# Kernel optimization log

Measured on AMD Instinct MI355X. Metric: run time of the kernel, lower is better.

The kernel has to match this reference:

```python
import jax, jax.numpy as jnp
import numpy as np

D = 1024
H = 16
HD = D // H
EPS = 1e-6


def setup_inputs() -> dict:
    key = jax.random.key(0)
    ks = jax.random.split(key, 10)
    s = 1.0 / np.sqrt(D)
    inp = {
        "x": jax.random.normal(ks[0], (2, 2048, D), dtype=jnp.float32),
        "Wq": jax.random.uniform(ks[1], (D, D), jnp.float32, -s, s),
        "bq": jax.random.uniform(ks[2], (D,), jnp.float32, -s, s),
        "Wk": jax.random.uniform(ks[3], (D, D), jnp.float32, -s, s),
        "bk": jax.random.uniform(ks[4], (D,), jnp.float32, -s, s),
        "Wv": jax.random.uniform(ks[5], (D, D), jnp.float32, -s, s),
        "bv": jax.random.uniform(ks[6], (D,), jnp.float32, -s, s),
        "Wo": jax.random.uniform(ks[7], (D, D), jnp.float32, -s, s),
        "bo": jax.random.uniform(ks[8], (D,), jnp.float32, -s, s),
        "gamma": jnp.ones((D,), jnp.float32),
        "beta": jnp.zeros((D,), jnp.float32),
    }
    return inp


def _mha(x, Wq, bq, Wk, bk, Wv, bv, Wo, bo, gamma, beta):
    B, S, _ = x.shape
    # Linear projections (torch Linear: x @ W.T + b), split heads -> [B,H,S,hd]
    q = (x @ Wq.T + bq).reshape(B, S, H, HD).transpose(0, 2, 1, 3)
    k = (x @ Wk.T + bk).reshape(B, S, H, HD).transpose(0, 2, 1, 3)
    v = (x @ Wv.T + bv).reshape(B, S, H, HD).transpose(0, 2, 1, 3)
    scores = jnp.einsum("bhqd,bhkd->bhqk", q, k) / jnp.sqrt(jnp.float32(HD))
    attn = jax.nn.softmax(scores, axis=-1)
    ctx = jnp.einsum("bhqk,bhkd->bhqd", attn, v)
    ctx = ctx.transpose(0, 2, 1, 3).reshape(B, S, D)
    out = ctx @ Wo.T + bo  # dropout p=0.0 -> identity
    res = x + out
    mu = jnp.mean(res, axis=-1, keepdims=True)
    var = jnp.mean(jnp.square(res - mu), axis=-1, keepdims=True)
    return (res - mu) / jnp.sqrt(var + EPS) * gamma + beta


def reference(x, Wq, bq, Wk, bk, Wv, bv, Wo, bo, gamma, beta):
    return _mha(x, Wq, bq, Wk, bk, Wv, bv, Wo, bo, gamma, beta)
```

## Files before the change

### kernel.cpp

```cpp
#include <hip/hip_runtime.h>
#include <hip/hip_bf16.h>
#include <math.h>

#define D_MODEL 1024
#define NH 16
#define HDIM 64
#define BB 2
#define SS 2048
#define MTOK (BB*SS)

typedef __hip_bfloat16 bf16;
typedef short s8v __attribute__((ext_vector_type(8)));
typedef float f4v __attribute__((ext_vector_type(4)));
typedef float f16v __attribute__((ext_vector_type(16)));

__device__ __forceinline__ float bf2f(bf16 x) { return __bfloat162float(x); }
__device__ __forceinline__ bf16 f2bf(float x) { return __float2bfloat16(x); }

typedef const __attribute__((address_space(1))) unsigned int* gas_u32;
typedef __attribute__((address_space(3))) unsigned int* las_u32;
#define ASYNC16(gp, lp) __builtin_amdgcn_global_load_lds((gas_u32)(gp), (las_u32)(lp), 16, 0, 0)

#define QSCALE 0.18033688f

__device__ __forceinline__ unsigned int cvtpk_bf16(float a, float b) {
    unsigned int r;
    asm("v_cvt_pk_bf16_f32 %0, %1, %2" : "=v"(r) : "v"(a), "v"(b));
    return r;
}

__global__ __launch_bounds__(256)
void cvt_kernel(const float* __restrict__ x,  const float* __restrict__ wq,
                const float* __restrict__ wk, const float* __restrict__ wv,
                const float* __restrict__ wo, bf16* __restrict__ dst)
{
    const size_t e = ((size_t)blockIdx.x * 256 + threadIdx.x) * 4;
    const size_t M1 = (size_t)1 << 20;
    const float* src; size_t off;
    if      (e < 4 * M1) { src = x;  off = e;          }
    else if (e < 5 * M1) { src = wq; off = e - 4 * M1; }
    else if (e < 6 * M1) { src = wk; off = e - 5 * M1; }
    else if (e < 7 * M1) { src = wv; off = e - 6 * M1; }
    else                 { src = wo; off = e - 7 * M1; }
    const float4 v = *(const float4*)&src[off];
    bf16 h[4] = { f2bf(v.x), f2bf(v.y), f2bf(v.z), f2bf(v.w) };
    *(uint2*)&dst[e] = *(const uint2*)h;
}

__global__ __launch_bounds__(256, 2)
void gemm_qkv(const bf16* __restrict__ X,
              const bf16* __restrict__ Wq, const float* __restrict__ bq,
              const bf16* __restrict__ Wk, const float* __restrict__ bk,
              const bf16* __restrict__ Wv, const float* __restrict__ bv,
              bf16* __restrict__ q_ws, bf16* __restrict__ k_ws, bf16* __restrict__ v_ws)
{
    const int mat = blockIdx.z;
    const bf16*  W    = (mat == 0) ? Wq : ((mat == 1) ? Wk : Wv);
    const float* bias = (mat == 0) ? bq : ((mat == 1) ? bk : bv);

    const int t = threadIdx.x;
    const int lane = t & 63, wave = t >> 6;
    const int wrow = wave >> 1, wcol = wave & 1;
    const int quad = lane >> 4, l15 = lane & 15;

    const bf16 *Ap, *Bp; int m0, n0;
    if (mat < 2) { Ap = X; Bp = W; m0 = blockIdx.y * 128; n0 = blockIdx.x * 128; }
    else         { Ap = W; Bp = X; m0 = blockIdx.x * 128; n0 = blockIdx.y * 128; }

    __shared__ __align__(16) bf16 As[128 * 64];
    __shared__ __align__(16) bf16 Bs[128 * 64];

    f4v acc[4][4];
#pragma unroll
    for (int i = 0; i < 4; i++)
#pragma unroll
        for (int j = 0; j < 4; j++) acc[i][j] = (f4v){0.f, 0.f, 0.f, 0.f};

    for (int kk = 0; kk < D_MODEL; kk += 64) {
#pragma unroll
        for (int p = 0; p < 4; p++) {
            const int c = p * 256 + t;
            const int row = c >> 3, j = c & 7;
            ASYNC16(&Ap[(size_t)(m0 + row) * D_MODEL + kk + (j ^ (row & 7)) * 8], &As[c * 8]);
        }
#pragma unroll
        for (int p = 0; p < 4; p++) {
            const int c = p * 256 + t;
            const int row = c >> 3, j = c & 7;
            ASYNC16(&Bp[(size_t)(n0 + row) * D_MODEL + kk + (j ^ (row & 7)) * 8], &Bs[c * 8]);
        }
        __syncthreads();

#pragma unroll
        for (int ks = 0; ks < 2; ks++) {
            s8v af[4], bf_[4];
#pragma unroll
            for (int i = 0; i < 4; i++) {
                const int row = wrow * 64 + i * 16 + l15;
                const int g = (ks * 4 + quad) ^ (row & 7);
                af[i] = *(const s8v*)&As[row * 64 + g * 8];
            }
#pragma unroll
            for (int j = 0; j < 4; j++) {
                const int row = wcol * 64 + j * 16 + l15;
                const int g = (ks * 4 + quad) ^ (row & 7);
                bf_[j] = *(const s8v*)&Bs[row * 64 + g * 8];
            }
#pragma unroll
            for (int i = 0; i < 4; i++)
#pragma unroll
                for (int j = 0; j < 4; j++)
                    acc[i][j] = __builtin_amdgcn_mfma_f32_16x16x32_bf16(af[i], bf_[j], acc[i][j], 0, 0, 0);
        }
        __syncthreads();
    }

    if (mat == 2) {
#pragma unroll
        for (int i = 0; i < 4; i++) {
#pragma unroll
            for (int r = 0; r < 4; r++) {
                const int f = m0 + wrow * 64 + i * 16 + quad * 4 + r;
                const float bv_ = bias[f];
#pragma unroll
                for (int j = 0; j < 4; j++) {
                    const int tok = n0 + wcol * 64 + j * 16 + l15;
                    const int b = tok >> 11, s = tok & 2047;
                    v_ws[((size_t)(b * D_MODEL + f)) * SS + s] = f2bf(acc[i][j][r] + bv_);
                }
            }
        }
    } else {
        bf16* dst = (mat == 0) ? q_ws : k_ws;
        const float scale = (mat == 0) ? QSCALE : 1.0f;
#pragma unroll
        for (int j = 0; j < 4; j++) {
            const int col = n0 + wcol * 64 + j * 16 + l15;
            const float bv_ = bias[col];
            const int h = col >> 6, hd = col & 63;
#pragma unroll
            for (int i = 0; i < 4; i++) {
#pragma unroll
                for (int r = 0; r < 4; r++) {
                    const int row = m0 + wrow * 64 + i * 16 + quad * 4 + r;
                    const int b = row >> 11, s = row & 2047;
                    const float v = (acc[i][j][r] + bv_) * scale;
                    dst[(((size_t)(b * NH + h)) * SS + s) * HDIM + hd] = f2bf(v);
                }
            }
        }
    }
}

__device__ __forceinline__ f16v qk_tile(const bf16* Ksc, const s8v* qf,
                                        const int mt, const int l31, const int L5)
{
    f16v sc;
#pragma unroll
    for (int i = 0; i < 16; i++) sc[i] = 0.f;
    __builtin_amdgcn_s_setprio(1);
#pragma unroll
    for (int kc = 0; kc < 4; kc++) {
        const int g = (kc * 2 + L5) ^ (l31 & 7);
        const s8v kf = *(const s8v*)&Ksc[(mt * 32 + l31) * 64 + g * 8];
        sc = __builtin_amdgcn_mfma_f32_32x32x16_bf16(kf, qf[kc], sc, 0, 0, 0);
    }
    __builtin_amdgcn_s_setprio(0);
    return sc;
}

__global__ __launch_bounds__(512, 4)
void attn_kernel(const bf16* __restrict__ Q, const bf16* __restrict__ K,
                 const bf16* __restrict__ VtG, bf16* __restrict__ ctx)
{
    const int s_ = blockIdx.x;
    const int lb = (s_ & 7) * 64 + (s_ >> 3);
    const int bh = lb >> 4;
    const int q0 = (lb & 15) * 128;
    const bf16* Qp = Q   + (size_t)bh * SS * HDIM;
    const bf16* Kp = K   + (size_t)bh * SS * HDIM;
    const bf16* Vp = VtG + (size_t)bh * HDIM * SS;

    __shared__ __align__(16) bf16 Qs[128 * 64];
    __shared__ __align__(16) bf16 Ks[2][128 * 64];
    __shared__ __align__(16) bf16 Vt[2][64 * 128];

    const int t = threadIdx.x;
    const int lane = t & 63, wave = t >> 6;
    const int l31 = lane & 31, L5 = lane >> 5;
    const int qb = (wave & 3) * 32;
    const int half = wave >> 2;

    const int vrbase = t >> 4;
    const int vcol = (t & 15) * 8;
    uint4 vv[2];
#pragma unroll
    for (int p = 0; p < 2; p++)
        vv[p] = *(const uint4*)&Vp[(size_t)(p * 32 + vrbase) * SS + vcol];
#pragma unroll
    for (int p = 0; p < 2; p++) {
        const int c = p * 512 + t;
        const int row = c >> 3, j = c & 7;
        ASYNC16(&Kp[(size_t)row * HDIM + (j ^ (row & 7)) * 8], &Ks[0][c * 8]);
    }
#pragma unroll
    for (int p = 0; p < 2; p++) {
        const int c = p * 512 + t;
        const int row = c >> 3, g = (c & 7) ^ (row & 7);
        *(uint4*)&Qs[row * 64 + g * 8] = *(const uint4*)&Qp[(size_t)(q0 + row) * HDIM + (c & 7) * 8];
    }
    const int cA = vcol,     pA = (cA & ~12) | ((cA & 4) << 1) | ((cA & 8) >> 1);
    const int cB = vcol + 4, pB = (cB & ~12) | ((cB & 4) << 1) | ((cB & 8) >> 1);
    {
        union { uint4 u4; uint2 u2[2]; } uu;
#pragma unroll
        for (int p = 0; p < 2; p++) {
            const int vr = p * 32 + vrbase;
            uu.u4 = vv[p];
            *(uint2*)&Vt[0][vr * 128 + (((pA >> 3) ^ (vr & 15)) * 8) + (pA & 7)] = uu.u2[0];
            *(uint2*)&Vt[0][vr * 128 + (((pB >> 3) ^ (vr & 15)) * 8) + (pB & 7)] = uu.u2[1];
        }
    }
    __syncthreads();

    s8v qf[4];
#pragma unroll
    for (int kc = 0; kc < 4; kc++) {
        const int g = (kc * 2 + L5) ^ (l31 & 7);
        qf[kc] = *(const s8v*)&Qs[(qb + l31) * 64 + g * 8];
    }

    float l_own = 0.f;
    f16v o_acc[2];
#pragma unroll
    for (int i = 0; i < 16; i++) { o_acc[0][i] = 0.f; o_acc[1][i] = 0.f; }

    int cur = 0;
    for (int it = 0; it < SS / 128; ++it) {
        const bool have = (it < SS / 128 - 1);
        const int s0n = (it + 1) * 128;

        uint4 nv0, nv1;
        if (have) {
            nv0 = *(const uint4*)&Vp[(size_t)(vrbase) * SS + s0n + vcol];
            nv1 = *(const uint4*)&Vp[(size_t)(32 + vrbase) * SS + s0n + vcol];
#pragma unroll
            for (int p = 0; p < 2; p++) {
                const int c = p * 512 + t;
                const int row = c >> 3, j = c & 7;
                ASYNC16(&Kp[(size_t)(s0n + row) * HDIM + (j ^ (row & 7)) * 8],
                        &Ks[cur ^ 1][c * 8]);
            }
        }

        const bf16* Ksc = &Ks[cur][0];
        const bf16* Vtc = &Vt[cur][0];
#pragma unroll
        for (int mt2 = 0; mt2 < 2; mt2++) {
            const int mt = half * 2 + mt2;
            f16v sc = qk_tile(Ksc, qf, mt, l31, L5);
            float tps = 0.f;
#pragma unroll
            for (int i = 0; i < 16; i++) { sc[i] = __builtin_amdgcn_exp2f(sc[i]); tps += sc[i]; }
            l_own += tps;
            unsigned int pk[8];
#pragma unroll
            for (int i = 0; i < 8; i++) pk[i] = cvtpk_bf16(sc[2 * i], sc[2 * i + 1]);
            __builtin_amdgcn_s_setprio(1);
#pragma unroll
            for (int c = 0; c < 2; c++) {
                const s8v pf = *(const s8v*)&pk[c * 4];
#pragma unroll
                for (int dt = 0; dt < 2; dt++) {
                    const int g = (mt * 4 + c * 2 + L5) ^ (l31 & 15);
                    const s8v vf = *(const s8v*)&Vtc[(dt * 32 + l31) * 128 + g * 8];
                    o_acc[dt] = __builtin_amdgcn_mfma_f32_32x32x16_bf16(pf, vf, o_acc[dt], 0, 0, 0);
                }
            }
            __builtin_amdgcn_s_setprio(0);
        }

        if (have) {
            bf16* VtN = &Vt[cur ^ 1][0];
            union { uint4 u4; uint2 u2[2]; } uu;
            const int vr0 = vrbase, vr1 = 32 + vrbase;
            uu.u4 = nv0;
            *(uint2*)&VtN[vr0 * 128 + (((pA >> 3) ^ (vr0 & 15)) * 8) + (pA & 7)] = uu.u2[0];
            *(uint2*)&VtN[vr0 * 128 + (((pB >> 3) ^ (vr0 & 15)) * 8) + (pB & 7)] = uu.u2[1];
            uu.u4 = nv1;
            *(uint2*)&VtN[vr1 * 128 + (((pA >> 3) ^ (vr1 & 15)) * 8) + (pA & 7)] = uu.u2[0];
            *(uint2*)&VtN[vr1 * 128 + (((pB >> 3) ^ (vr1 & 15)) * 8) + (pB & 7)] = uu.u2[1];
        }
        __syncthreads();
        cur ^= 1;
    }

    const float l_wave = l_own + __shfl_xor(l_own, 32);
    float* o_sh = (float*)&Ks[0][0];
    float* l_sh = (float*)&Vt[0][0];
    if (half == 1) {
        const int pr = wave & 3;
#pragma unroll
        for (int dt = 0; dt < 2; dt++)
#pragma unroll
            for (int reg = 0; reg < 16; reg++)
                o_sh[((pr * 2 + dt) * 16 + reg) * 64 + lane] = o_acc[dt][reg];
        if (lane < 32) l_sh[pr * 32 + l31] = l_wave;
    }
    __syncthreads();
    if (half == 0) {
        const int pr = wave;
        const float linv = 1.0f / (l_wave + l_sh[pr * 32 + l31]);
        const int b = bh >> 4, h = bh & 15;
#pragma unroll
        for (int reg = 0; reg < 16; reg++) {
            const int R = (reg & 3) + 8 * (reg >> 2) + 4 * L5;
            const float lr = __shfl(linv, R);
            const int tok = q0 + qb + R;
            const size_t rb = ((size_t)(b * SS + tok)) * D_MODEL + h * 64;
#pragma unroll
            for (int dt = 0; dt < 2; dt++) {
                const float val = o_acc[dt][reg] + o_sh[((pr * 2 + dt) * 16 + reg) * 64 + lane];
                ctx[rb + dt * 32 + l31] = f2bf(val * lr);
            }
        }
    }
}

__global__ __launch_bounds__(256, 2)
void gemm_oproj(const bf16* __restrict__ Ctx, const bf16* __restrict__ Wo,
                const float* __restrict__ bo, const float* __restrict__ X,
                float* __restrict__ res)
{
    const int m0 = blockIdx.y * 128, n0 = blockIdx.x * 128;
    const int t = threadIdx.x;
    const int lane = t & 63, wave = t >> 6;
    const int wrow = wave >> 1, wcol = wave & 1;
    const int quad = lane >> 4, l15 = lane & 15;

    __shared__ __align__(16) bf16 As[128 * 64];
    __shared__ __align__(16) bf16 Bs[128 * 64];

    f4v acc[4][4];
#pragma unroll
    for (int i = 0; i < 4; i++)
#pragma unroll
        for (int j = 0; j < 4; j++) acc[i][j] = (f4v){0.f, 0.f, 0.f, 0.f};

    for (int kk = 0; kk < D_MODEL; kk += 64) {
#pragma unroll
        for (int p = 0; p < 4; p++) {
            const int c = p * 256 + t;
            const int row = c >> 3, j = c & 7;
            ASYNC16(&Ctx[(size_t)(m0 + row) * D_MODEL + kk + (j ^ (row & 7)) * 8], &As[c * 8]);
        }
#pragma unroll
        for (int p = 0; p < 4; p++) {
            const int c = p * 256 + t;
            const int row = c >> 3, j = c & 7;
            ASYNC16(&Wo[(size_t)(n0 + row) * D_MODEL + kk + (j ^ (row & 7)) * 8], &Bs[c * 8]);
        }
        __syncthreads();

#pragma unroll
        for (int ks = 0; ks < 2; ks++) {
            s8v af[4], bf_[4];
#pragma unroll
            for (int i = 0; i < 4; i++) {
                const int row = wrow * 64 + i * 16 + l15;
                const int g = (ks * 4 + quad) ^ (row & 7);
                af[i] = *(const s8v*)&As[row * 64 + g * 8];
            }
#pragma unroll
            for (int j = 0; j < 4; j++) {
                const int row = wcol * 64 + j * 16 + l15;
                const int g = (ks * 4 + quad) ^ (row & 7);
                bf_[j] = *(const s8v*)&Bs[row * 64 + g * 8];
            }
#pragma unroll
            for (int i = 0; i < 4; i++)
#pragma unroll
                for (int j = 0; j < 4; j++)
                    acc[i][j] = __builtin_amdgcn_mfma_f32_16x16x32_bf16(af[i], bf_[j], acc[i][j], 0, 0, 0);
        }
        __syncthreads();
    }

#pragma unroll
    for (int j = 0; j < 4; j++) {
        const int col = n0 + wcol * 64 + j * 16 + l15;
        const float bv_ = bo[col];
#pragma unroll
        for (int i = 0; i < 4; i++) {
#pragma unroll
            for (int r = 0; r < 4; r++) {
                const int row = m0 + wrow * 64 + i * 16 + quad * 4 + r;
                const size_t idx = (size_t)row * D_MODEL + col;
                res[idx] = acc[i][j][r] + bv_ + X[idx];
            }
        }
    }
}

__global__ __launch_bounds__(256)
void ln_kernel(const float* __restrict__ res, const float* __restrict__ gamma,
               const float* __restrict__ beta, float* __restrict__ out)
{
    const int row = blockIdx.x;
    const int t = threadIdx.x;
    const float4 v = *(const float4*)&res[(size_t)row * D_MODEL + t * 4];

    float s = v.x + v.y + v.z + v.w;
    float sq = v.x * v.x + v.y * v.y + v.z * v.z + v.w * v.w;
#pragma unroll
    for (int m = 1; m < 64; m <<= 1) {
        s += __shfl_xor(s, m);
        sq += __shfl_xor(sq, m);
    }
    __shared__ float red[8];
    const int wave = t >> 6, lane = t & 63;
    if (lane == 0) { red[wave] = s; red[4 + wave] = sq; }
    __syncthreads();
    s = red[0] + red[1] + red[2] + red[3];
    sq = red[4] + red[5] + red[6] + red[7];
    const float mu = s * (1.0f / D_MODEL);
    const float var = sq * (1.0f / D_MODEL) - mu * mu;
    const float rstd = rsqrtf(var + 1e-6f);

    const float vv[4] = {v.x, v.y, v.z, v.w};
    float4 o;
    o.x = (vv[0] - mu) * rstd * gamma[t * 4 + 0] + beta[t * 4 + 0];
    o.y = (vv[1] - mu) * rstd * gamma[t * 4 + 1] + beta[t * 4 + 1];
    o.z = (vv[2] - mu) * rstd * gamma[t * 4 + 2] + beta[t * 4 + 2];
    o.w = (vv[3] - mu) * rstd * gamma[t * 4 + 3] + beta[t * 4 + 3];
    *(float4*)&out[(size_t)row * D_MODEL + t * 4] = o;
}

extern "C" void kernel_launch(void* const* d_in, const int* in_sizes, int n_in,
                              void* d_out, int out_size, void* d_ws, size_t ws_size,
                              hipStream_t stream) {
    const float* x     = (const float*)d_in[0];
    const float* Wq    = (const float*)d_in[1];
    const float* bq    = (const float*)d_in[2];
    const float* Wk    = (const float*)d_in[3];
    const float* bk    = (const float*)d_in[4];
    const float* Wv    = (const float*)d_in[5];
    const float* bv    = (const float*)d_in[6];
    const float* Wo    = (const float*)d_in[7];
    const float* bo    = (const float*)d_in[8];
    const float* gamma = (const float*)d_in[9];
    const float* beta  = (const float*)d_in[10];
    float* out = (float*)d_out;

    char* ws = (char*)d_ws;
    bf16* xb  = (bf16*)(ws);
    bf16* Wqb = (bf16*)(ws + ((size_t)8 << 20));
    bf16* Wkb = (bf16*)(ws + ((size_t)10 << 20));
    bf16* Wvb = (bf16*)(ws + ((size_t)12 << 20));
    bf16* Wob = (bf16*)(ws + ((size_t)14 << 20));
    bf16*  q_ws   = (bf16*)(ws + ((size_t)16 << 20));
    bf16*  k_ws   = (bf16*)(ws + ((size_t)24 << 20));
    bf16*  v_ws   = (bf16*)(ws + ((size_t)32 << 20));
    bf16*  ctx_ws = (bf16*)(ws + ((size_t)40 << 20));
    float* res_ws = (float*)(ws + ((size_t)16 << 20));

    cvt_kernel<<<8192, 256, 0, stream>>>(x, Wq, Wk, Wv, Wo, xb);
    gemm_qkv<<<dim3(8, 32, 3), 256, 0, stream>>>(xb, Wqb, bq, Wkb, bk, Wvb, bv, q_ws, k_ws, v_ws);
    attn_kernel<<<512, 512, 0, stream>>>(q_ws, k_ws, v_ws, ctx_ws);
    gemm_oproj<<<dim3(8, 32), 256, 0, stream>>>(ctx_ws, Wob, bo, x, res_ws);
    ln_kernel<<<MTOK, 256, 0, stream>>>(res_ws, gamma, beta, out);
}
```

Measured before the change: 200.1 us.

## Fuse fp32-to-bf16 conversion into GEMM tile loads, drop separate convert kernel

Removes the standalone conversion kernel and has the QKV and output-projection GEMMs load fp32 inputs and weights directly, converting to bf16 in registers before writing swizzled tiles to LDS. This saves a kernel launch plus a full write and re-read of the bf16 copies. In exchange, the GEMMs read twice as many bytes per tile, redo the conversion in every block that shares a tile, and replace the async global-to-LDS loads with synchronous register-staged loads, which can expose latency.

```diff
diff --git a/kernel.cpp b/kernel.cpp
--- a/kernel.cpp
+++ b/kernel.cpp
@@ -14,7 +14,6 @@
 typedef float f4v __attribute__((ext_vector_type(4)));
 typedef float f16v __attribute__((ext_vector_type(16)));
 
-__device__ __forceinline__ float bf2f(bf16 x) { return __bfloat162float(x); }
 __device__ __forceinline__ bf16 f2bf(float x) { return __float2bfloat16(x); }
 
 typedef const __attribute__((address_space(1))) unsigned int* gas_u32;
@@ -29,33 +28,26 @@
     return r;
 }
 
-__global__ __launch_bounds__(256)
-void cvt_kernel(const float* __restrict__ x,  const float* __restrict__ wq,
-                const float* __restrict__ wk, const float* __restrict__ wv,
-                const float* __restrict__ wo, bf16* __restrict__ dst)
-{
-    const size_t e = ((size_t)blockIdx.x * 256 + threadIdx.x) * 4;
-    const size_t M1 = (size_t)1 << 20;
-    const float* src; size_t off;
-    if      (e < 4 * M1) { src = x;  off = e;          }
-    else if (e < 5 * M1) { src = wq; off = e - 4 * M1; }
-    else if (e < 6 * M1) { src = wk; off = e - 5 * M1; }
-    else if (e < 7 * M1) { src = wv; off = e - 6 * M1; }
-    else                 { src = wo; off = e - 7 * M1; }
-    const float4 v = *(const float4*)&src[off];
-    bf16 h[4] = { f2bf(v.x), f2bf(v.y), f2bf(v.z), f2bf(v.w) };
-    *(uint2*)&dst[e] = *(const uint2*)h;
+__device__ __forceinline__ uint4 ld_cvt8(const float* p) {
+    const float4 f0 = *(const float4*)p;
+    const float4 f1 = *(const float4*)(p + 4);
+    uint4 u;
+    u.x = cvtpk_bf16(f0.x, f0.y);
+    u.y = cvtpk_bf16(f0.z, f0.w);
+    u.z = cvtpk_bf16(f1.x, f1.y);
+    u.w = cvtpk_bf16(f1.z, f1.w);
+    return u;
 }
 
 __global__ __launch_bounds__(256, 2)
-void gemm_qkv(const bf16* __restrict__ X,
-              const bf16* __restrict__ Wq, const float* __restrict__ bq,
-              const bf16* __restrict__ Wk, const float* __restrict__ bk,
-              const bf16* __restrict__ Wv, const float* __restrict__ bv,
+void gemm_qkv(const float* __restrict__ X,
+              const float* __restrict__ Wq, const float* __restrict__ bq,
+              const float* __restrict__ Wk, const float* __restrict__ bk,
+              const float* __restrict__ Wv, const float* __restrict__ bv,
               bf16* __restrict__ q_ws, bf16* __restrict__ k_ws, bf16* __restrict__ v_ws)
 {
     const int mat = blockIdx.z;
-    const bf16*  W    = (mat == 0) ? Wq : ((mat == 1) ? Wk : Wv);
+    const float* W    = (mat == 0) ? Wq : ((mat == 1) ? Wk : Wv);
     const float* bias = (mat == 0) ? bq : ((mat == 1) ? bk : bv);
 
     const int t = threadIdx.x;
@@ -63,7 +55,7 @@
     const int wrow = wave >> 1, wcol = wave & 1;
     const int quad = lane >> 4, l15 = lane & 15;
 
-    const bf16 *Ap, *Bp; int m0, n0;
+    const float *Ap, *Bp; int m0, n0;
     if (mat < 2) { Ap = X; Bp = W; m0 = blockIdx.y * 128; n0 = blockIdx.x * 128; }
     else         { Ap = W; Bp = X; m0 = blockIdx.x * 128; n0 = blockIdx.y * 128; }
 
@@ -81,13 +73,15 @@
         for (int p = 0; p < 4; p++) {
             const int c = p * 256 + t;
             const int row = c >> 3, j = c & 7;
-            ASYNC16(&Ap[(size_t)(m0 + row) * D_MODEL + kk + (j ^ (row & 7)) * 8], &As[c * 8]);
+            const uint4 u = ld_cvt8(&Ap[(size_t)(m0 + row) * D_MODEL + kk + j * 8]);
+            *(uint4*)&As[row * 64 + (j ^ (row & 7)) * 8] = u;
         }
 #pragma unroll
         for (int p = 0; p < 4; p++) {
             const int c = p * 256 + t;
             const int row = c >> 3, j = c & 7;
-            ASYNC16(&Bp[(size_t)(n0 + row) * D_MODEL + kk + (j ^ (row & 7)) * 8], &Bs[c * 8]);
+            const uint4 u = ld_cvt8(&Bp[(size_t)(n0 + row) * D_MODEL + kk + j * 8]);
+            *(uint4*)&Bs[row * 64 + (j ^ (row & 7)) * 8] = u;
         }
         __syncthreads();
 
@@ -328,7 +322,7 @@
 }
 
 __global__ __launch_bounds__(256, 2)
-void gemm_oproj(const bf16* __restrict__ Ctx, const bf16* __restrict__ Wo,
+void gemm_oproj(const bf16* __restrict__ Ctx, const float* __restrict__ Wo,
                 const float* __restrict__ bo, const float* __restrict__ X,
                 float* __restrict__ res)
 {
@@ -358,7 +352,8 @@
         for (int p = 0; p < 4; p++) {
             const int c = p * 256 + t;
             const int row = c >> 3, j = c & 7;
-            ASYNC16(&Wo[(size_t)(n0 + row) * D_MODEL + kk + (j ^ (row & 7)) * 8], &Bs[c * 8]);
+            const uint4 u = ld_cvt8(&Wo[(size_t)(n0 + row) * D_MODEL + kk + j * 8]);
+            *(uint4*)&Bs[row * 64 + (j ^ (row & 7)) * 8] = u;
         }
         __syncthreads();
 
@@ -453,20 +448,14 @@
     float* out = (float*)d_out;
 
     char* ws = (char*)d_ws;
-    bf16* xb  = (bf16*)(ws);
-    bf16* Wqb = (bf16*)(ws + ((size_t)8 << 20));
-    bf16* Wkb = (bf16*)(ws + ((size_t)10 << 20));
-    bf16* Wvb = (bf16*)(ws + ((size_t)12 << 20));
-    bf16* Wob = (bf16*)(ws + ((size_t)14 << 20));
     bf16*  q_ws   = (bf16*)(ws + ((size_t)16 << 20));
     bf16*  k_ws   = (bf16*)(ws + ((size_t)24 << 20));
     bf16*  v_ws   = (bf16*)(ws + ((size_t)32 << 20));
     bf16*  ctx_ws = (bf16*)(ws + ((size_t)40 << 20));
     float* res_ws = (float*)(ws + ((size_t)16 << 20));
 
-    cvt_kernel<<<8192, 256, 0, stream>>>(x, Wq, Wk, Wv, Wo, xb);
-    gemm_qkv<<<dim3(8, 32, 3), 256, 0, stream>>>(xb, Wqb, bq, Wkb, bk, Wvb, bv, q_ws, k_ws, v_ws);
+    gemm_qkv<<<dim3(8, 32, 3), 256, 0, stream>>>(x, Wq, bq, Wk, bk, Wv, bv, q_ws, k_ws, v_ws);
     attn_kernel<<<512, 512, 0, stream>>>(q_ws, k_ws, v_ws, ctx_ws);
-    gemm_oproj<<<dim3(8, 32), 256, 0, stream>>>(ctx_ws, Wob, bo, x, res_ws);
+    gemm_oproj<<<dim3(8, 32), 256, 0, stream>>>(ctx_ws, Wo, bo, x, res_ws);
     ln_kernel<<<MTOK, 256, 0, stream>>>(res_ws, gamma, beta, out);
 }
```

Result: slower. 227.2 us (+13.6%).
